# Kernel optimization log

Measured on AMD Instinct MI355X. Metric: run time of the kernel, lower is better.

## Reference

```python
import jax, jax.numpy as jnp
import numpy as np

B, C, T, H, W = 1024, 1, 500, 7, 7
HID, OUT = 16, 2


def setup_inputs() -> dict:
    key = jax.random.key(0)
    k1, k2, k3, k4 = jax.random.split(key, 4)
    rppg_embeddings = jax.random.normal(k1, (B, C, T, H, W), dtype=jnp.float32)
    rBr = jax.random.normal(k2, (B, C, T), dtype=jnp.float32)
    # final_dense_layer params: Linear(500,16) -> Dropout (identity at eval) -> Linear(16,2)
    W1 = jax.random.normal(k3, (C * T, HID), dtype=jnp.float32) / np.sqrt(C * T)
    b1 = jnp.zeros((HID,), dtype=jnp.float32)
    W2 = jax.random.normal(k4, (HID, OUT), dtype=jnp.float32) / np.sqrt(HID)
    b2 = jnp.zeros((OUT,), dtype=jnp.float32)
    return {"rppg_embeddings": rppg_embeddings, "rBr": rBr,
            "W1": W1, "b1": b1, "W2": W2, "b2": b2}


def reference(rppg_embeddings, rBr, W1, b1, W2, b2):
    # AvgPool3d(kernel=[1,7,7], stride=1, pad=0) on (B,C,T,7,7) -> (B,C,T,1,1):
    # equivalent to mean over the full 7x7 spatial window.
    x = jnp.mean(rppg_embeddings, axis=(-2, -1))            # (B, C, T)
    # batched FFT phase along time (replaces the per-(b,c) Python loop)
    phase = jnp.angle(jnp.fft.fft(x, axis=-1))              # (B, C, T)
    flat = phase.reshape(phase.shape[0], -1)                # (B, C*T) = (B, 500)
    h = flat @ W1 + b1                                      # (B, 16); dropout = identity (eval)
    rBP = h @ W2 + b2                                       # (B, 2)
    return rBP
```

## Files before the change

### kernel.cpp

```cpp
#include <hip/hip_runtime.h>
#include <math.h>

#ifndef M_PI
#define M_PI 3.14159265358979323846
#endif

#define T_LEN 500
#define HW49  49
#define HID   16
#define NOUT  2

__global__ __launch_bounds__(256) void pool_kernel(
    const float* __restrict__ rppg, float* __restrict__ xout)
{
    __shared__ __align__(16) float stage[6272];
    const int tid   = threadIdx.x;
    const int row   = blockIdx.x >> 2;
    const int chunk = blockIdx.x & 3;
    const int bin0  = chunk * 128;
    const int bins  = (bin0 + 128 <= T_LEN) ? 128 : (T_LEN - bin0);
    const int nv4   = (bins * HW49) >> 2;
    const float* src = rppg + (size_t)row * (T_LEN * HW49) + bin0 * HW49;
    const float4* s4 = (const float4*)src;
    float4* st4 = (float4*)stage;
    for (int i = tid; i < nv4; i += 256) st4[i] = s4[i];
    __syncthreads();
    if (tid < bins) {
        float acc = 0.f;
        const float* p = stage + tid * HW49;
        #pragma unroll
        for (int j = 0; j < HW49; ++j) acc += p[j];
        xout[row * T_LEN + bin0 + tid] = acc * (1.0f / 49.0f);
    }
}

__global__ __launch_bounds__(256, 4) void dft_head_kernel(
    const float* __restrict__ xin,
    const float* __restrict__ W1,
    const float* __restrict__ b1,
    const float* __restrict__ W2,
    const float* __restrict__ b2,
    float* __restrict__ out)
{
    __shared__ __align__(16) double xd[T_LEN];
    __shared__ float hred[256 * 17];
    const int tid = threadIdx.x;
    const int row = blockIdx.x;

    const float* xr = xin + (size_t)row * T_LEN;
    for (int i = tid; i < T_LEN; i += 256) xd[i] = (double)xr[i];
    __syncthreads();

    float hp[HID];
    #pragma unroll
    for (int j = 0; j < HID; ++j) hp[j] = 0.f;

    if (tid <= 250) {
        const int k = tid;
        float ph;
        if (k == 250) {
            ph = 0.0f;
        } else {
            const double ang = (double)k * (-2.0 * M_PI / 500.0);
            double c1, s1;
            sincos(ang, &s1, &c1);
            const double c2 = fma(c1, c1, -(s1 * s1));
            const double s2 = 2.0 * c1 * s1;
            const double c4 = fma(c2, c2, -(s2 * s2));
            const double s4 = 2.0 * c2 * s2;
            const double c3 = fma(c1, c2, -(s1 * s2));
            const double s3 = fma(c1, s2,  (s1 * c2));

            double cw = 1.0, sw = 0.0;
            double re0 = 0.0, im0 = 0.0, re1 = 0.0, im1 = 0.0;
            double re2 = 0.0, im2 = 0.0, re3 = 0.0, im3 = 0.0;
            const double2* x2 = (const double2*)xd;
            for (int j = 0; j < 125; ++j) {
                const double2 xa = x2[2 * j];
                const double2 xb = x2[2 * j + 1];
                re0 = fma(xa.x, cw, re0); im0 = fma(xa.x, sw, im0);
                re1 = fma(xa.y, cw, re1); im1 = fma(xa.y, sw, im1);
                re2 = fma(xb.x, cw, re2); im2 = fma(xb.x, sw, im2);
                re3 = fma(xb.y, cw, re3); im3 = fma(xb.y, sw, im3);
                const double tc = fma(cw, c4, -(sw * s4));
                sw = fma(cw, s4, sw * c4);
                cw = tc;
            }
            const double re = re0 + (fma(c1, re1, -(s1 * im1)))
                                  + (fma(c2, re2, -(s2 * im2)))
                                  + (fma(c3, re3, -(s3 * im3)));
            const double im = im0 + (fma(c1, im1,  (s1 * re1)))
                                  + (fma(c2, im2,  (s2 * re2)))
                                  + (fma(c3, im3,  (s3 * re3)));
            ph = (float)atan2(im, re);
        }

        if (k == 0 || k == 250) {
            const float* w = W1 + k * HID;
            #pragma unroll
            for (int j = 0; j < HID; ++j) hp[j] = ph * w[j];
        } else {
            const float* wa = W1 + k * HID;
            const float* wb = W1 + (T_LEN - k) * HID;
            #pragma unroll
            for (int j = 0; j < HID; ++j) hp[j] = ph * (wa[j] - wb[j]);
        }
    }

    __syncthreads();
    #pragma unroll
    for (int j = 0; j < HID; ++j) hred[tid * 17 + j] = hp[j];
    __syncthreads();
    for (int sft = 128; sft >= 1; sft >>= 1) {
        if (tid < sft) {
            #pragma unroll
            for (int j = 0; j < HID; ++j)
                hred[tid * 17 + j] += hred[(tid + sft) * 17 + j];
        }
        __syncthreads();
    }

    if (tid < NOUT) {
        const int o = tid;
        float acc = b2[o];
        #pragma unroll
        for (int j = 0; j < HID; ++j)
            acc = fmaf(hred[j] + b1[j], W2[j * NOUT + o], acc);
        out[row * NOUT + o] = acc;
    }
}

__global__ __launch_bounds__(256, 4) void bp_head_fused_kernel(
    const float* __restrict__ rppg,
    const float* __restrict__ W1, const float* __restrict__ b1,
    const float* __restrict__ W2, const float* __restrict__ b2,
    float* __restrict__ out)
{
    __shared__ __align__(16) float stage[6272];
    __shared__ __align__(16) float xsh[T_LEN];
    const int tid = threadIdx.x;
    const int b   = blockIdx.x;
    const float* src = rppg + (size_t)b * (T_LEN * HW49);

    for (int c = 0; c < 4; ++c) {
        const int bin0 = c * 128;
        const int bins = (bin0 + 128 <= T_LEN) ? 128 : (T_LEN - bin0);
        const int nv4  = (bins * HW49) >> 2;
        const float4* s4 = (const float4*)(src + bin0 * HW49);
        float4* st4 = (float4*)stage;
        for (int i = tid; i < nv4; i += 256) st4[i] = s4[i];
        __syncthreads();
        if (tid < bins) {
            float acc = 0.f;
            const float* p = stage + tid * HW49;
            #pragma unroll
            for (int j = 0; j < HW49; ++j) acc += p[j];
            xsh[bin0 + tid] = acc * (1.0f / 49.0f);
        }
        __syncthreads();
    }

    float hp[HID];
    #pragma unroll
    for (int j = 0; j < HID; ++j) hp[j] = 0.f;

    if (tid <= 250) {
        const int k = tid;
        float ph;
        if (k == 250) {
            ph = 0.0f;
        } else {
            const double ang = (double)k * (-2.0 * M_PI / 500.0);
            double c1, s1;
            sincos(ang, &s1, &c1);
            const double c2 = fma(c1, c1, -(s1 * s1));
            const double s2 = 2.0 * c1 * s1;
            const double c4 = fma(c2, c2, -(s2 * s2));
            const double s4 = 2.0 * c2 * s2;
            const double c3 = fma(c1, c2, -(s1 * s2));
            const double s3 = fma(c1, s2,  (s1 * c2));
            double cw = 1.0, sw = 0.0;
            double re0 = 0, im0 = 0, re1 = 0, im1 = 0, re2 = 0, im2 = 0, re3 = 0, im3 = 0;
            const float4* x4 = (const float4*)xsh;
            for (int j = 0; j < 125; ++j) {
                const float4 xv = x4[j];
                const double x0 = (double)xv.x, x1 = (double)xv.y;
                const double x2v = (double)xv.z, x3 = (double)xv.w;
                re0 = fma(x0, cw, re0); im0 = fma(x0, sw, im0);
                re1 = fma(x1, cw, re1); im1 = fma(x1, sw, im1);
                re2 = fma(x2v, cw, re2); im2 = fma(x2v, sw, im2);
                re3 = fma(x3, cw, re3); im3 = fma(x3, sw, im3);
                const double tc = fma(cw, c4, -(sw * s4));
                sw = fma(cw, s4, sw * c4);
                cw = tc;
            }
            const double re = re0 + (fma(c1, re1, -(s1 * im1)))
                                  + (fma(c2, re2, -(s2 * im2)))
                                  + (fma(c3, re3, -(s3 * im3)));
            const double im = im0 + (fma(c1, im1,  (s1 * re1)))
                                  + (fma(c2, im2,  (s2 * re2)))
                                  + (fma(c3, im3,  (s3 * re3)));
            ph = (float)atan2(im, re);
        }
        if (k == 0 || k == 250) {
            const float* w = W1 + k * HID;
            #pragma unroll
            for (int j = 0; j < HID; ++j) hp[j] = ph * w[j];
        } else {
            const float* wa = W1 + k * HID;
            const float* wb = W1 + (T_LEN - k) * HID;
            #pragma unroll
            for (int j = 0; j < HID; ++j) hp[j] = ph * (wa[j] - wb[j]);
        }
    }

    __syncthreads();
    float* hred = stage;
    #pragma unroll
    for (int j = 0; j < HID; ++j) hred[tid * 17 + j] = hp[j];
    __syncthreads();
    for (int sft = 128; sft >= 1; sft >>= 1) {
        if (tid < sft) {
            #pragma unroll
            for (int j = 0; j < HID; ++j)
                hred[tid * 17 + j] += hred[(tid + sft) * 17 + j];
        }
        __syncthreads();
    }
    if (tid < NOUT) {
        const int o = tid;
        float acc = b2[o];
        #pragma unroll
        for (int j = 0; j < HID; ++j)
            acc = fmaf(hred[j] + b1[j], W2[j * NOUT + o], acc);
        out[b * NOUT + o] = acc;
    }
}

extern "C" void kernel_launch(void* const* d_in, const int* in_sizes, int n_in,
                              void* d_out, int out_size, void* d_ws, size_t ws_size,
                              hipStream_t stream) {
    const float* rppg = (const float*)d_in[0];
    const float* W1 = (const float*)d_in[2];
    const float* b1 = (const float*)d_in[3];
    const float* W2 = (const float*)d_in[4];
    const float* b2 = (const float*)d_in[5];
    float* out = (float*)d_out;

    const size_t need = (size_t)1024 * T_LEN * sizeof(float);
    if (ws_size >= need) {
        float* x = (float*)d_ws;
        pool_kernel<<<dim3(4096), dim3(256), 0, stream>>>(rppg, x);
        dft_head_kernel<<<dim3(1024), dim3(256), 0, stream>>>(x, W1, b1, W2, b2, out);
    } else {
        bp_head_fused_kernel<<<dim3(1024), dim3(256), 0, stream>>>(rppg, W1, b1, W2, b2, out);
    }
}
```

Measured before the change: 174.7 us.

## Split DFT time axis across two half-blocks and combine partial sums

The DFT head kernel now runs with 512 threads. Each frequency bin's 500-point sum is split into two 250-sample halves computed by separate threads, and the second half's partial result is exchanged through shared memory. It is combined using the (-1)^k twiddle, since the half offset of 250 samples equals half the period. This halves the serial FP64 loop length per thread and doubles threads per row, at the cost of an extra barrier, more shared memory, and redundant sincos calls. Launch bounds are changed to (512, 8).

```diff
diff --git a/kernel.cpp b/kernel.cpp
--- a/kernel.cpp
+++ b/kernel.cpp
@@ -34,7 +34,7 @@
     }
 }
 
-__global__ __launch_bounds__(256, 4) void dft_head_kernel(
+__global__ __launch_bounds__(512, 8) void dft_head_kernel(
     const float* __restrict__ xin,
     const float* __restrict__ W1,
     const float* __restrict__ b1,
@@ -42,75 +42,93 @@
     const float* __restrict__ b2,
     float* __restrict__ out)
 {
-    __shared__ __align__(16) double xd[T_LEN];
+    __shared__ __align__(16) double  xd[512];
+    __shared__ __align__(16) double2 pairbuf[256];
     __shared__ float hred[256 * 17];
     const int tid = threadIdx.x;
     const int row = blockIdx.x;
-
     const float* xr = xin + (size_t)row * T_LEN;
-    for (int i = tid; i < T_LEN; i += 256) xd[i] = (double)xr[i];
-    __syncthreads();
-
-    float hp[HID];
-    #pragma unroll
-    for (int j = 0; j < HID; ++j) hp[j] = 0.f;
-
-    if (tid <= 250) {
-        const int k = tid;
-        float ph;
-        if (k == 250) {
-            ph = 0.0f;
-        } else {
-            const double ang = (double)k * (-2.0 * M_PI / 500.0);
-            double c1, s1;
-            sincos(ang, &s1, &c1);
-            const double c2 = fma(c1, c1, -(s1 * s1));
-            const double s2 = 2.0 * c1 * s1;
-            const double c4 = fma(c2, c2, -(s2 * s2));
-            const double s4 = 2.0 * c2 * s2;
-            const double c3 = fma(c1, c2, -(s1 * s2));
-            const double s3 = fma(c1, s2,  (s1 * c2));
-
-            double cw = 1.0, sw = 0.0;
-            double re0 = 0.0, im0 = 0.0, re1 = 0.0, im1 = 0.0;
-            double re2 = 0.0, im2 = 0.0, re3 = 0.0, im3 = 0.0;
-            const double2* x2 = (const double2*)xd;
-            for (int j = 0; j < 125; ++j) {
-                const double2 xa = x2[2 * j];
-                const double2 xb = x2[2 * j + 1];
-                re0 = fma(xa.x, cw, re0); im0 = fma(xa.x, sw, im0);
-                re1 = fma(xa.y, cw, re1); im1 = fma(xa.y, sw, im1);
-                re2 = fma(xb.x, cw, re2); im2 = fma(xb.x, sw, im2);
-                re3 = fma(xb.y, cw, re3); im3 = fma(xb.y, sw, im3);
-                const double tc = fma(cw, c4, -(sw * s4));
-                sw = fma(cw, s4, sw * c4);
-                cw = tc;
-            }
-            const double re = re0 + (fma(c1, re1, -(s1 * im1)))
-                                  + (fma(c2, re2, -(s2 * im2)))
-                                  + (fma(c3, re3, -(s3 * im3)));
-            const double im = im0 + (fma(c1, im1,  (s1 * re1)))
-                                  + (fma(c2, im2,  (s2 * re2)))
-                                  + (fma(c3, im3,  (s3 * re3)));
+
+    {
+        double v;
+        if      (tid < 250) v = (double)xr[tid];
+        else if (tid < 252) v = 0.0;
+        else if (tid < 502) v = (double)xr[tid - 2];
+        else                v = 0.0;
+        xd[tid] = v;
+    }
+    __syncthreads();
+
+    const bool isA = (tid < 256);
+    const int  k   = isA ? tid : (tid - 256);
+
+    double Xre = 0.0, Xim = 0.0;
+    double ang = 0.0;
+    if (k <= 249) {
+        ang = (double)k * (-2.0 * M_PI / 500.0);
+        double c1, s1;
+        sincos(ang, &s1, &c1);
+        const double c2 = fma(c1, c1, -(s1 * s1));
+        const double s2 = 2.0 * c1 * s1;
+        const double c4 = fma(c2, c2, -(s2 * s2));
+        const double s4 = 2.0 * c2 * s2;
+
+        const double2* bp = ((const double2*)xd) + (isA ? 0 : 126);
+        double cw = 1.0, sw = 0.0;
+        double re0 = 0, im0 = 0, re1 = 0, im1 = 0;
+        double re2 = 0, im2 = 0, re3 = 0, im3 = 0;
+        double2 xa = bp[0], xb = bp[1];
+        for (int j = 0; j < 63; ++j) {
+            const double2 na = bp[2 * j + 2];
+            const double2 nb = bp[2 * j + 3];
+            re0 = fma(xa.x, cw, re0); im0 = fma(xa.x, sw, im0);
+            re1 = fma(xa.y, cw, re1); im1 = fma(xa.y, sw, im1);
+            re2 = fma(xb.x, cw, re2); im2 = fma(xb.x, sw, im2);
+            re3 = fma(xb.y, cw, re3); im3 = fma(xb.y, sw, im3);
+            const double tc = fma(cw, c4, -(sw * s4));
+            sw = fma(cw, s4, sw * c4);
+            cw = tc;
+            xa = na; xb = nb;
+        }
+        double c1b, s1b;
+        sincos(ang, &s1b, &c1b);
+        const double c2b = fma(c1b, c1b, -(s1b * s1b));
+        const double s2b = 2.0 * c1b * s1b;
+        const double c3b = fma(c1b, c2b, -(s1b * s2b));
+        const double s3b = fma(c1b, s2b,  (s1b * c2b));
+        Xre = re0 + fma(c1b, re1, -(s1b * im1))
+                  + fma(c2b, re2, -(s2b * im2))
+                  + fma(c3b, re3, -(s3b * im3));
+        Xim = im0 + fma(c1b, im1,  (s1b * re1))
+                  + fma(c2b, im2,  (s2b * re2))
+                  + fma(c3b, im3,  (s3b * re3));
+    }
+
+    if (!isA && k <= 249) pairbuf[k] = double2{Xre, Xim};
+    __syncthreads();
+
+    if (isA) {
+        float ph = 0.0f;
+        if (k <= 249) {
+            const double2 Bv = pairbuf[k];
+            const double sgn = (k & 1) ? -1.0 : 1.0;
+            const double re = fma(sgn, Bv.x, Xre);
+            const double im = fma(sgn, Bv.y, Xim);
             ph = (float)atan2(im, re);
         }
-
-        if (k == 0 || k == 250) {
+        if (k == 0 || k >= 250) {
             const float* w = W1 + k * HID;
             #pragma unroll
-            for (int j = 0; j < HID; ++j) hp[j] = ph * w[j];
+            for (int j = 0; j < HID; ++j) hred[k * 17 + j] = ph * w[j];
         } else {
             const float* wa = W1 + k * HID;
             const float* wb = W1 + (T_LEN - k) * HID;
             #pragma unroll
-            for (int j = 0; j < HID; ++j) hp[j] = ph * (wa[j] - wb[j]);
-        }
-    }
-
-    __syncthreads();
-    #pragma unroll
-    for (int j = 0; j < HID; ++j) hred[tid * 17 + j] = hp[j];
-    __syncthreads();
+            for (int j = 0; j < HID; ++j) hred[k * 17 + j] = ph * (wa[j] - wb[j]);
+        }
+    }
+    __syncthreads();
+
     for (int sft = 128; sft >= 1; sft >>= 1) {
         if (tid < sft) {
             #pragma unroll
@@ -251,7 +269,7 @@
     if (ws_size >= need) {
         float* x = (float*)d_ws;
         pool_kernel<<<dim3(4096), dim3(256), 0, stream>>>(rppg, x);
-        dft_head_kernel<<<dim3(1024), dim3(256), 0, stream>>>(x, W1, b1, W2, b2, out);
+        dft_head_kernel<<<dim3(1024), dim3(512), 0, stream>>>(x, W1, b1, W2, b2, out);
     } else {
         bp_head_fused_kernel<<<dim3(1024), dim3(256), 0, stream>>>(rppg, W1, b1, W2, b2, out);
     }
```

New measurement: 176.4 us. Within noise of the previous version (+1.0%).
